# Kernel tuning notes

Hardware: AMD Instinct MI355X
Metric: run time of the kernel (lower is better)

Reference implementation:

```python
import jax, jax.numpy as jnp
import numpy as np

B, T, D, K = 64, 512, 1024, 32


def setup_inputs() -> dict:
    key = jax.random.key(0)
    ks = jax.random.split(key, 6)
    vectors = jax.random.normal(ks[0], (B, T, D), dtype=jnp.float32)
    mask = jnp.ones((B, T), dtype=jnp.int32)
    targets = jax.random.randint(ks[1], (B, T), 0, K, dtype=jnp.int32)
    W = jax.random.normal(ks[2], (K, D), dtype=jnp.float32) * 0.02
    b = jnp.zeros((K,), dtype=jnp.float32)
    transitions = jax.random.normal(ks[3], (K, K), dtype=jnp.float32) * 0.01
    start_trans = jax.random.normal(ks[4], (K,), dtype=jnp.float32) * 0.01
    end_trans = jax.random.normal(ks[5], (K,), dtype=jnp.float32) * 0.01
    return {"vectors": vectors, "mask": mask, "targets": targets, "W": W,
            "b": b, "transitions": transitions, "start_trans": start_trans,
            "end_trans": end_trans}


def _crf_loglik(logits, tags, maskf, transitions, start_trans, end_trans):
    # logits: [B,T,K], tags: [B,T] int, maskf: [B,T] float
    # ---- partition function via forward algorithm (logsumexp semiring scan) ----
    alpha0 = start_trans[None, :] + logits[:, 0]  # [B,K]

    def step(alpha, xs):
        logit_t, m_t = xs  # [B,K], [B]
        # inner[b,i,j] = alpha[b,i] + transitions[i,j] + logit_t[b,j]
        inner = alpha[:, :, None] + transitions[None, :, :] + logit_t[:, None, :]
        new_alpha = jax.nn.logsumexp(inner, axis=1)  # [B,K]
        alpha = jnp.where(m_t[:, None] > 0, new_alpha, alpha)
        return alpha, None

    logits_t = jnp.swapaxes(logits, 0, 1)  # [T,B,K]
    mask_t = jnp.swapaxes(maskf, 0, 1)     # [T,B]
    alpha, _ = jax.lax.scan(step, alpha0, (logits_t[1:], mask_t[1:]))
    partition = jax.nn.logsumexp(alpha + end_trans[None, :], axis=-1)  # [B]

    # ---- joint score of the gold tag sequence ----
    emit = jnp.take_along_axis(logits, tags[..., None], axis=-1)[..., 0]  # [B,T]
    emit_score = jnp.sum(emit[:, :-1] * maskf[:, :-1], axis=1)            # [B]
    trans_score = jnp.sum(transitions[tags[:, :-1], tags[:, 1:]] * maskf[:, 1:], axis=1)
    last_idx = jnp.sum(maskf, axis=1).astype(jnp.int32) - 1  # [B]
    last_tags = jnp.take_along_axis(tags, last_idx[:, None], axis=1)[:, 0]
    score = (start_trans[tags[:, 0]] + emit_score + trans_score
             + end_trans[last_tags] + emit[:, -1] * maskf[:, -1])
    return jnp.sum(score - partition)  # summed log-likelihood over batch


def reference(vectors, mask, targets, W, b, transitions, start_trans, end_trans):
    logits = jnp.einsum("btd,kd->btk", vectors, W) + b  # [B,T,K]
    maskf = mask.astype(logits.dtype)
    loglik = _crf_loglik(logits, targets.astype(jnp.int32), maskf,
                         transitions, start_trans, end_trans)
    loss = -loglik / jnp.sum(maskf)
    return loss, logits
```

## Files before the change

### kernel.cpp

```cpp
#include <hip/hip_runtime.h>
#include <hip/hip_bf16.h>

#define Bz 64
#define Tz 512
#define Dz 1024
#define Kz 32

#define MOFF 128
#define LOFF (128 + 1024 * 1024)

typedef __attribute__((ext_vector_type(8)))  __bf16 bf16x8;
typedef __attribute__((ext_vector_type(16))) float  f32x16;

__device__ __forceinline__ float bcast_lane(float x, int i) {
    return __uint_as_float(__builtin_amdgcn_readlane(__float_as_uint(x), i));
}

__device__ __forceinline__ unsigned pack2bf(float lo, float hi) {
    return __builtin_amdgcn_perm(__float_as_uint(hi) + 0x8000u,
                                 __float_as_uint(lo) + 0x8000u, 0x07060302u);
}

union BfCast { unsigned u[4]; bf16x8 v; };

__global__ __launch_bounds__(256) void logits_kernel(
        const float* __restrict__ V, const float* __restrict__ W,
        const float* __restrict__ bias, float* __restrict__ out) {
    __shared__ float part[3][16][64];

    const int tid  = threadIdx.x;
    const int wv   = tid >> 6;
    const int lane = tid & 63;
    const int n    = lane & 31;
    const int h    = lane >> 5;
    const int r0   = blockIdx.x * 32;

    const float* arow = V + (size_t)(r0 + n) * Dz + wv * 256 + h * 8;

    float4 pf[4][2];
    #pragma unroll
    for (int s = 0; s < 4; ++s) {
        pf[s][0] = *(const float4*)(arow + s * 16);
        pf[s][1] = *(const float4*)(arow + s * 16 + 4);
    }

    const float* wrow = W + (size_t)n * Dz + wv * 256 + h * 8;
    BfCast wf[16];
    #pragma unroll
    for (int kb = 0; kb < 16; ++kb) {
        const float4 w0 = *(const float4*)(wrow + kb * 16);
        const float4 w1 = *(const float4*)(wrow + kb * 16 + 4);
        wf[kb].u[0] = pack2bf(w0.x, w0.y);
        wf[kb].u[1] = pack2bf(w0.z, w0.w);
        wf[kb].u[2] = pack2bf(w1.x, w1.y);
        wf[kb].u[3] = pack2bf(w1.z, w1.w);
    }

    f32x16 acc;
    #pragma unroll
    for (int i = 0; i < 16; ++i) acc[i] = 0.f;

    #pragma unroll
    for (int kb = 0; kb < 16; ++kb) {
        const float4 a0 = pf[kb & 3][0];
        const float4 a1 = pf[kb & 3][1];
        if (kb + 4 < 16) {
            pf[kb & 3][0] = *(const float4*)(arow + (kb + 4) * 16);
            pf[kb & 3][1] = *(const float4*)(arow + (kb + 4) * 16 + 4);
        }
        BfCast cA;
        cA.u[0] = pack2bf(a0.x, a0.y);
        cA.u[1] = pack2bf(a0.z, a0.w);
        cA.u[2] = pack2bf(a1.x, a1.y);
        cA.u[3] = pack2bf(a1.z, a1.w);
        acc = __builtin_amdgcn_mfma_f32_32x32x16_bf16(cA.v, wf[kb].v, acc, 0, 0, 0);
    }

    if (wv > 0) {
        #pragma unroll
        for (int i = 0; i < 16; ++i) part[wv - 1][i][lane] = acc[i];
    }
    __syncthreads();
    if (wv == 0) {
        const float bv = bias[n];
        #pragma unroll
        for (int i = 0; i < 16; ++i) {
            const float s = ((acc[i] + part[0][i][lane]) +
                             (part[1][i][lane] + part[2][i][lane])) + bv;
            const int row = (i & 3) + 8 * (i >> 2) + 4 * h;
            out[(size_t)(r0 + row) * Kz + n] = s;
        }
    }
}

__global__ __launch_bounds__(64) void crf_seg_kernel(
        const float* __restrict__ logits, const float* __restrict__ trans,
        float* __restrict__ ws) {
    __shared__ float xpose[33 * 32];

    const int bid  = blockIdx.x;
    const int b    = bid >> 4;
    const int seg  = bid & 15;
    const int lane = threadIdx.x;
    const int n    = lane & 31;
    const int h    = lane >> 5;

    int rIdx[16];
    #pragma unroll
    for (int i = 0; i < 16; ++i) rIdx[i] = (i & 3) + 8 * (i >> 2) + 4 * h;

    float etf[16];
    #pragma unroll
    for (int i = 0; i < 16; ++i) etf[i] = __expf(trans[rIdx[i] * Kz + n]);

    const float* lg = logits + ((size_t)b * Tz + (size_t)seg * 32) * Kz;
    float Ev[32];
    #pragma unroll
    for (int u = 0; u < 32; ++u) Ev[u] = __expf(lg[u * Kz + n]);

    unsigned bu[8];
    #pragma unroll
    for (int q = 0; q < 4; ++q) {
        bu[q] = ((rIdx[2 * q] == n) ? 0x3F80u : 0u) |
                (((rIdx[2 * q + 1] == n) ? 0x3F80u : 0u) << 16);
        bu[4 + q] = ((rIdx[8 + 2 * q] == n) ? 0x3F80u : 0u) |
                    (((rIdx[8 + 2 * q + 1] == n) ? 0x3F80u : 0u) << 16);
    }

    f32x16 zf;
    #pragma unroll
    for (int i = 0; i < 16; ++i) zf[i] = 0.f;

    float Xs[16];
    #pragma unroll
    for (int i = 0; i < 16; ++i) Xs[i] = (rIdx[i] == n) ? 1.f : 0.f;
    float lsc = 0.f;

    #pragma unroll
    for (int u = 0; u < 32; ++u) {
        if (u > 0 || seg > 0) {
            const float E = Ev[u];
            BfCast cA1, cA2, cB1, cB2;
            #pragma unroll
            for (int q = 0; q < 4; ++q) {
                cA1.u[q] = pack2bf(E * etf[2 * q], E * etf[2 * q + 1]);
                cA2.u[q] = pack2bf(E * etf[8 + 2 * q], E * etf[8 + 2 * q + 1]);
                cB1.u[q] = bu[q];
                cB2.u[q] = bu[4 + q];
            }
            f32x16 acc = __builtin_amdgcn_mfma_f32_32x32x16_bf16(cA1.v, cB1.v, zf, 0, 0, 0);
            acc = __builtin_amdgcn_mfma_f32_32x32x16_bf16(cA2.v, cB2.v, acc, 0, 0, 0);
            #pragma unroll
            for (int i = 0; i < 16; ++i) Xs[i] = acc[i];
            if ((u & 7) == 7) {
                float m = Xs[0];
                #pragma unroll
                for (int i = 1; i < 16; ++i) m = fmaxf(m, Xs[i]);
                #pragma unroll
                for (int dd = 1; dd < 64; dd <<= 1) m = fmaxf(m, __shfl_xor(m, dd, 64));
                const float r = __builtin_amdgcn_rcpf(m);
                lsc += __logf(m);
                #pragma unroll
                for (int i = 0; i < 16; ++i) Xs[i] *= r;
            }
            #pragma unroll
            for (int q = 0; q < 4; ++q) {
                bu[q]     = pack2bf(Xs[2 * q], Xs[2 * q + 1]);
                bu[4 + q] = pack2bf(Xs[8 + 2 * q], Xs[8 + 2 * q + 1]);
            }
        }
    }

    #pragma unroll
    for (int i = 0; i < 16; ++i)
        xpose[n * 33 + rIdx[i]] = Xs[i];
    __syncthreads();
    float* mout = ws + MOFF + (size_t)bid * 1024;
    #pragma unroll
    for (int k = 0; k < 16; ++k) {
        const int row = 2 * k + h;
        mout[row * 32 + n] = xpose[row * 33 + n];
    }
    if (lane == 0) ws[LOFF + bid] = lsc;
}

__global__ __launch_bounds__(64) void crf_combine_kernel(
        const float* __restrict__ logits, const int* __restrict__ mask,
        const int* __restrict__ targets, const float* __restrict__ trans,
        const float* __restrict__ start_t, const float* __restrict__ end_t,
        float* __restrict__ ws) {
    const int b    = blockIdx.x;
    const int lane = threadIdx.x;
    const int n    = lane & 31;

    const float* lg = logits + (size_t)b * Tz * Kz;
    const int*   tg = targets + b * Tz;
    const int*   mk = mask + b * Tz;

    float emit_s = 0.f, trans_s = 0.f, msum = 0.f;
    for (int t = lane; t < Tz; t += 64) {
        const int   tt = tg[t];
        const float m  = (float)mk[t];
        emit_s += lg[t * Kz + tt] * m;
        if (t > 0) trans_s += trans[tg[t - 1] * Kz + tt] * m;
        msum += m;
    }
    float ssum = emit_s + trans_s;
    #pragma unroll
    for (int dd = 1; dd < 64; dd <<= 1) {
        ssum += __shfl_xor(ssum, dd, 64);
        msum += __shfl_xor(msum, dd, 64);
    }

    float al = start_t[n] + lg[n];
    float m0 = al;
    #pragma unroll
    for (int dd = 1; dd < 32; dd <<= 1) m0 = fmaxf(m0, __shfl_xor(m0, dd, 64));
    float v    = __expf(al - m0);
    float lacc = m0;

    const float* Pb = ws + MOFF + (size_t)b * 16 * 1024;
    float pv[32];
    #pragma unroll
    for (int i = 0; i < 32; ++i) pv[i] = Pb[i * 32 + n];

    #pragma unroll
    for (int s = 0; s < 16; ++s) {
        float pn[32];
        if (s + 1 < 16) {
            const float* Pn = Pb + (size_t)(s + 1) * 1024;
            #pragma unroll
            for (int i = 0; i < 32; ++i) pn[i] = Pn[i * 32 + n];
        }
        float n0 = 0.f, n1 = 0.f, n2 = 0.f, n3 = 0.f;
        #pragma unroll
        for (int i = 0; i < 32; i += 4) {
            n0 = fmaf(bcast_lane(v, i + 0), pv[i + 0], n0);
            n1 = fmaf(bcast_lane(v, i + 1), pv[i + 1], n1);
            n2 = fmaf(bcast_lane(v, i + 2), pv[i + 2], n2);
            n3 = fmaf(bcast_lane(v, i + 3), pv[i + 3], n3);
        }
        v = (n0 + n1) + (n2 + n3);
        lacc += ws[LOFF + b * 16 + s];
        float mm = v;
        #pragma unroll
        for (int dd = 1; dd < 32; dd <<= 1) mm = fmaxf(mm, __shfl_xor(mm, dd, 64));
        v *= __builtin_amdgcn_rcpf(mm);
        lacc += __logf(mm);
        if (s + 1 < 16) {
            #pragma unroll
            for (int i = 0; i < 32; ++i) pv[i] = pn[i];
        }
    }

    float w  = v * __expf(end_t[n]);
    float sv = w;
    #pragma unroll
    for (int dd = 1; dd < 32; dd <<= 1) sv += __shfl_xor(sv, dd, 64);
    const float part = lacc + __logf(sv);

    if (lane == 0) {
        const int lastIdx = (int)msum - 1;
        const float score = start_t[tg[0]] + ssum + end_t[tg[lastIdx]];
        ws[b]      = score - part;
        ws[64 + b] = msum;
    }
}

__global__ __launch_bounds__(64) void crf_final_kernel(
        const float* __restrict__ ws, float* __restrict__ out) {
    const int lane = threadIdx.x;
    float p    = ws[lane];
    float msum = ws[64 + lane];
    #pragma unroll
    for (int dd = 1; dd < 64; dd <<= 1) {
        p    += __shfl_xor(p, dd, 64);
        msum += __shfl_xor(msum, dd, 64);
    }
    if (lane == 0) out[0] = -p / msum;
}

extern "C" void kernel_launch(void* const* d_in, const int* in_sizes, int n_in,
                              void* d_out, int out_size, void* d_ws, size_t ws_size,
                              hipStream_t stream) {
    const float* V       = (const float*)d_in[0];
    const int*   mask    = (const int*)d_in[1];
    const int*   targets = (const int*)d_in[2];
    const float* W       = (const float*)d_in[3];
    const float* bias    = (const float*)d_in[4];
    const float* trans   = (const float*)d_in[5];
    const float* start_t = (const float*)d_in[6];
    const float* end_t   = (const float*)d_in[7];

    float* out = (float*)d_out;
    float* ws  = (float*)d_ws;

    logits_kernel<<<1024, 256, 0, stream>>>(V, W, bias, out + 1);
    crf_seg_kernel<<<1024, 64, 0, stream>>>(out + 1, trans, ws);
    crf_combine_kernel<<<64, 64, 0, stream>>>(out + 1, mask, targets, trans,
                                              start_t, end_t, ws);
    crf_final_kernel<<<1, 64, 0, stream>>>(ws, out);
}
```

Baseline: 243.8 us.

## Fuse logits GEMM with CRF segment scan and preload segment log-scales

Merges the logits kernel and the per-segment CRF matrix-product kernel into one launch. Wave 0 of each block reuses the freshly reduced logits, with their exponentials staged in shared memory, to run the 32-step segment scan, instead of re-reading logits from global memory in a separate kernel. The combine kernel also loads the 16 per-segment log-scales once and broadcasts them across lanes instead of reading global memory each step. The trade-off is that three of the four waves in each block sit idle during the serial scan, and the extra shared memory may reduce occupancy.

```diff
diff --git a/kernel.cpp b/kernel.cpp
--- a/kernel.cpp
+++ b/kernel.cpp
@@ -23,17 +23,21 @@
 
 union BfCast { unsigned u[4]; bf16x8 v; };
 
-__global__ __launch_bounds__(256) void logits_kernel(
+__global__ __launch_bounds__(256, 3) void logits_seg_kernel(
         const float* __restrict__ V, const float* __restrict__ W,
-        const float* __restrict__ bias, float* __restrict__ out) {
+        const float* __restrict__ bias, const float* __restrict__ trans,
+        float* __restrict__ out, float* __restrict__ ws) {
     __shared__ float part[3][16][64];
+    __shared__ float evs[32 * 32];
+    __shared__ float xpose[33 * 32];
 
     const int tid  = threadIdx.x;
     const int wv   = tid >> 6;
     const int lane = tid & 63;
     const int n    = lane & 31;
     const int h    = lane >> 5;
-    const int r0   = blockIdx.x * 32;
+    const int bid  = blockIdx.x;
+    const int r0   = bid * 32;
 
     const float* arow = V + (size_t)(r0 + n) * Dz + wv * 256 + h * 8;
 
@@ -81,42 +85,31 @@
         for (int i = 0; i < 16; ++i) part[wv - 1][i][lane] = acc[i];
     }
     __syncthreads();
-    if (wv == 0) {
-        const float bv = bias[n];
-        #pragma unroll
-        for (int i = 0; i < 16; ++i) {
-            const float s = ((acc[i] + part[0][i][lane]) +
-                             (part[1][i][lane] + part[2][i][lane])) + bv;
-            const int row = (i & 3) + 8 * (i >> 2) + 4 * h;
-            out[(size_t)(r0 + row) * Kz + n] = s;
-        }
-    }
-}
-
-__global__ __launch_bounds__(64) void crf_seg_kernel(
-        const float* __restrict__ logits, const float* __restrict__ trans,
-        float* __restrict__ ws) {
-    __shared__ float xpose[33 * 32];
-
-    const int bid  = blockIdx.x;
-    const int b    = bid >> 4;
-    const int seg  = bid & 15;
-    const int lane = threadIdx.x;
-    const int n    = lane & 31;
-    const int h    = lane >> 5;
+    if (wv != 0) return;
 
     int rIdx[16];
     #pragma unroll
     for (int i = 0; i < 16; ++i) rIdx[i] = (i & 3) + 8 * (i >> 2) + 4 * h;
 
+    const float bv = bias[n];
+    #pragma unroll
+    for (int i = 0; i < 16; ++i) {
+        const float s = ((acc[i] + part[0][i][lane]) +
+                         (part[1][i][lane] + part[2][i][lane])) + bv;
+        out[(size_t)(r0 + rIdx[i]) * Kz + n] = s;
+        evs[rIdx[i] * 32 + n] = __expf(s);
+    }
+    __builtin_amdgcn_wave_barrier();
+
+    const int seg = bid & 15;
+
     float etf[16];
     #pragma unroll
     for (int i = 0; i < 16; ++i) etf[i] = __expf(trans[rIdx[i] * Kz + n]);
 
-    const float* lg = logits + ((size_t)b * Tz + (size_t)seg * 32) * Kz;
     float Ev[32];
     #pragma unroll
-    for (int u = 0; u < 32; ++u) Ev[u] = __expf(lg[u * Kz + n]);
+    for (int u = 0; u < 32; ++u) Ev[u] = evs[u * 32 + n];
 
     unsigned bu[8];
     #pragma unroll
@@ -148,10 +141,10 @@
                 cB1.u[q] = bu[q];
                 cB2.u[q] = bu[4 + q];
             }
-            f32x16 acc = __builtin_amdgcn_mfma_f32_32x32x16_bf16(cA1.v, cB1.v, zf, 0, 0, 0);
-            acc = __builtin_amdgcn_mfma_f32_32x32x16_bf16(cA2.v, cB2.v, acc, 0, 0, 0);
-            #pragma unroll
-            for (int i = 0; i < 16; ++i) Xs[i] = acc[i];
+            f32x16 a2 = __builtin_amdgcn_mfma_f32_32x32x16_bf16(cA1.v, cB1.v, zf, 0, 0, 0);
+            a2 = __builtin_amdgcn_mfma_f32_32x32x16_bf16(cA2.v, cB2.v, a2, 0, 0, 0);
+            #pragma unroll
+            for (int i = 0; i < 16; ++i) Xs[i] = a2[i];
             if ((u & 7) == 7) {
                 float m = Xs[0];
                 #pragma unroll
@@ -174,7 +167,7 @@
     #pragma unroll
     for (int i = 0; i < 16; ++i)
         xpose[n * 33 + rIdx[i]] = Xs[i];
-    __syncthreads();
+    __builtin_amdgcn_wave_barrier();
     float* mout = ws + MOFF + (size_t)bid * 1024;
     #pragma unroll
     for (int k = 0; k < 16; ++k) {
@@ -197,6 +190,8 @@
     const int*   tg = targets + b * Tz;
     const int*   mk = mask + b * Tz;
 
+    float lscv = (lane < 16) ? ws[LOFF + b * 16 + lane] : 0.f;
+
     float emit_s = 0.f, trans_s = 0.f, msum = 0.f;
     for (int t = lane; t < Tz; t += 64) {
         const int   tt = tg[t];
@@ -241,7 +236,7 @@
             n3 = fmaf(bcast_lane(v, i + 3), pv[i + 3], n3);
         }
         v = (n0 + n1) + (n2 + n3);
-        lacc += ws[LOFF + b * 16 + s];
+        lacc += bcast_lane(lscv, s);
         float mm = v;
         #pragma unroll
         for (int dd = 1; dd < 32; dd <<= 1) mm = fmaxf(mm, __shfl_xor(mm, dd, 64));
@@ -295,8 +290,7 @@
     float* out = (float*)d_out;
     float* ws  = (float*)d_ws;
 
-    logits_kernel<<<1024, 256, 0, stream>>>(V, W, bias, out + 1);
-    crf_seg_kernel<<<1024, 64, 0, stream>>>(out + 1, trans, ws);
+    logits_seg_kernel<<<1024, 256, 0, stream>>>(V, W, bias, trans, out + 1, ws);
     crf_combine_kernel<<<64, 64, 0, stream>>>(out + 1, mask, targets, trans,
                                               start_t, end_t, ws);
     crf_final_kernel<<<1, 64, 0, stream>>>(ws, out);
```

New measurement: 235.8 us. 1.03x faster.
